# Performance work log

Measured on AMD Instinct MI355X. Metric: run time of the kernel, lower is better.

Reference implementation:

```python
import jax, jax.numpy as jnp
import numpy as np

N = 100000      # nodes
E = 800000      # edges
F_IN = 128      # input feature dim
HID = 8         # per-head hidden
HEADS = 8
HD = HID * HEADS  # 64
G = 128         # graphs in batch
C = 10          # classes
SLOPE = 0.2     # leaky relu negative slope


def setup_inputs() -> dict:
    key = jax.random.key(0)
    ks = iter(jax.random.split(key, 48))
    def rn(shape, scale=0.1):
        return jax.random.normal(next(ks), shape, jnp.float32) * scale
    inp = {
        'x': jax.random.normal(next(ks), (N, F_IN), jnp.float32),
        'edge_index': jax.random.randint(next(ks), (2, E), 0, N),
        'batch': jnp.sort(jax.random.randint(next(ks), (N,), 0, G)),
        # GAT layer 1
        'W1': rn((F_IN, HEADS * HID)), 'as1': rn((HEADS, HID)), 'ad1': rn((HEADS, HID)), 'b1': jnp.zeros((HEADS * HID,), jnp.float32),
        # GAT layer 2
        'W2': rn((HD, HEADS * HID)), 'as2': rn((HEADS, HID)), 'ad2': rn((HEADS, HID)), 'b2': jnp.zeros((HEADS * HID,), jnp.float32),
        # node attention MLP (HD -> HD//2 -> 2)
        'na_w1': rn((HD, HD // 2)), 'na_b1': jnp.zeros((HD // 2,), jnp.float32), 'na_w2': rn((HD // 2, 2)), 'na_b2': jnp.zeros((2,), jnp.float32),
        # edge attention MLP (2*HD -> HD -> 2)
        'ea_w1': rn((2 * HD, HD)), 'ea_b1': jnp.zeros((HD,), jnp.float32), 'ea_w2': rn((HD, 2)), 'ea_b2': jnp.zeros((2,), jnp.float32),
        # GCN causal / trivial
        'gc_w': rn((HD, HD)), 'gc_b': jnp.zeros((HD,), jnp.float32),
        'gt_w': rn((HD, HD)), 'gt_b': jnp.zeros((HD,), jnp.float32),
        # readouts
        'rc_w': rn((HD, HD)), 'rc_b': jnp.zeros((HD,), jnp.float32),
        'rt_w': rn((HD, HD)), 'rt_b': jnp.zeros((HD,), jnp.float32),
        # classifiers (HD -> HD//2 -> C), combined (2HD -> HD -> C)
        'cc_w1': rn((HD, HD // 2)), 'cc_b1': jnp.zeros((HD // 2,), jnp.float32), 'cc_w2': rn((HD // 2, C)), 'cc_b2': jnp.zeros((C,), jnp.float32),
        'ct_w1': rn((HD, HD // 2)), 'ct_b1': jnp.zeros((HD // 2,), jnp.float32), 'ct_w2': rn((HD // 2, C)), 'ct_b2': jnp.zeros((C,), jnp.float32),
        'cm_w1': rn((2 * HD, HD)), 'cm_b1': jnp.zeros((HD,), jnp.float32), 'cm_w2': rn((HD, C)), 'cm_b2': jnp.zeros((C,), jnp.float32),
    }
    return inp


def _mlp2(h, w1, b1, w2, b2):
    return jax.nn.relu(h @ w1 + b1) @ w2 + b2


def reference(x, edge_index, batch,
              W1, as1, ad1, b1, W2, as2, ad2, b2,
              na_w1, na_b1, na_w2, na_b2,
              ea_w1, ea_b1, ea_w2, ea_b2,
              gc_w, gc_b, gt_w, gt_b,
              rc_w, rc_b, rt_w, rt_b,
              cc_w1, cc_b1, cc_w2, cc_b2,
              ct_w1, ct_b1, ct_w2, ct_b2,
              cm_w1, cm_b1, cm_w2, cm_b2):
    src, dst = edge_index[0], edge_index[1]
    loop = jnp.arange(N)
    s2 = jnp.concatenate([src, loop])  # edges + self-loops (PyG GATConv/GCNConv add self-loops)
    d2 = jnp.concatenate([dst, loop])

    def gat(h_in, W, a_s, a_d, b):
        h = (h_in @ W).reshape(N, HEADS, HID)
        es = jnp.einsum('nhd,hd->nh', h, a_s)
        ed = jnp.einsum('nhd,hd->nh', h, a_d)
        logit = jax.nn.leaky_relu(es[s2] + ed[d2], SLOPE)      # [E+N, H]
        m = jax.ops.segment_max(logit, d2, num_segments=N)
        ex = jnp.exp(logit - m[d2])
        den = jax.ops.segment_sum(ex, d2, num_segments=N)
        alpha = ex / (den[d2] + 1e-16)
        out = jax.ops.segment_sum(h[s2] * alpha[..., None], d2, num_segments=N)
        return out.reshape(N, HEADS * HID) + b

    # GNN encoder (dropout disabled: eval mode)
    H1 = jax.nn.elu(gat(x, W1, as1, ad1, b1))
    H = gat(H1, W2, as2, ad2, b2)                              # [N, HD]

    # node attention
    na = jax.nn.softmax(_mlp2(H, na_w1, na_b1, na_w2, na_b2), axis=1)
    alpha_c, alpha_t = na[:, 0], na[:, 1]
    # edge attention (original edges, no self-loops)
    ef = jnp.concatenate([H[src], H[dst]], axis=1)             # [E, 2*HD]
    ea = jax.nn.softmax(_mlp2(ef, ea_w1, ea_b1, ea_w2, ea_b2), axis=1)
    beta_c, beta_t = ea[:, 0], ea[:, 1]

    Hc = H * alpha_c[:, None]
    Ht = H * alpha_t[:, None]

    def gcn(h_in, w, b, ew):
        # PyG gcn_norm: self-loops with weight 1, symmetric deg^-1/2 normalization
        w_full = jnp.concatenate([ew, jnp.ones((N,), h_in.dtype)])
        deg = jax.ops.segment_sum(w_full, d2, num_segments=N)
        dis = jnp.where(deg > 0, jax.lax.rsqrt(jnp.maximum(deg, 1e-20)), 0.0)
        norm = dis[s2] * w_full * dis[d2]
        h = h_in @ w
        return jax.ops.segment_sum(h[s2] * norm[:, None], d2, num_segments=N) + b

    Gc = gcn(Hc, gc_w, gc_b, beta_c)
    Gt = gcn(Ht, gt_w, gt_b, beta_t)

    # readout: linear then global_add_pool
    hGc = jax.ops.segment_sum(Gc @ rc_w + rc_b, batch, num_segments=G)  # [G, HD]
    hGt = jax.ops.segment_sum(Gt @ rt_w + rt_b, batch, num_segments=G)

    zc = _mlp2(hGc, cc_w1, cc_b1, cc_w2, cc_b2)
    zt = _mlp2(hGt, ct_w1, ct_b1, ct_w2, ct_b2)
    # RandomIntervention: within-graph node shuffle followed by add-pool == plain add-pool
    h_comb = jnp.concatenate([hGc + hGt], axis=1) if False else (hGc + hGt)
    zp = _mlp2(jnp.concatenate([h_comb, jnp.zeros_like(h_comb)], axis=1), cm_w1, cm_b1, cm_w2, cm_b2) if False else _mlp2_comb(h_comb, cm_w1, cm_b1, cm_w2, cm_b2)
    return (zc, zt, zp, hGc, hGt)


def _mlp2_comb(h_comb, cm_w1, cm_b1, cm_w2, cm_b2):
    # original: classifier_combined takes hidden_dim*2 input; forward feeds h_G_c + shuffled_h_G_t
    # which is [G, HD]; to match Linear(2*HD, ...) we use the first HD rows of cm_w1 twice?
    # NO -- the original code as written passes a [G, HD] tensor to a Linear(2*HD, HD) layer,
    # which would error in torch. Faithful runnable interpretation: combined feature is
    # concat([h_G_c, shuffled_h_G_t]) of width 2*HD (the standard CAL formulation).
    return jax.nn.relu(h_comb @ cm_w1 + cm_b1) @ cm_w2 + cm_b2


# clean final definition overriding the commented exploration above
def reference(x, edge_index, batch,
              W1, as1, ad1, b1, W2, as2, ad2, b2,
              na_w1, na_b1, na_w2, na_b2,
              ea_w1, ea_b1, ea_w2, ea_b2,
              gc_w, gc_b, gt_w, gt_b,
              rc_w, rc_b, rt_w, rt_b,
              cc_w1, cc_b1, cc_w2, cc_b2,
              ct_w1, ct_b1, ct_w2, ct_b2,
              cm_w1, cm_b1, cm_w2, cm_b2):
    src, dst = edge_index[0], edge_index[1]
    loop = jnp.arange(N)
    s2 = jnp.concatenate([src, loop])
    d2 = jnp.concatenate([dst, loop])

    def gat(h_in, W, a_s, a_d, b):
        h = (h_in @ W).reshape(N, HEADS, HID)
        es = jnp.einsum('nhd,hd->nh', h, a_s)
        ed = jnp.einsum('nhd,hd->nh', h, a_d)
        logit = jax.nn.leaky_relu(es[s2] + ed[d2], SLOPE)
        m = jax.ops.segment_max(logit, d2, num_segments=N)
        ex = jnp.exp(logit - m[d2])
        den = jax.ops.segment_sum(ex, d2, num_segments=N)
        alpha = ex / (den[d2] + 1e-16)
        out = jax.ops.segment_sum(h[s2] * alpha[..., None], d2, num_segments=N)
        return out.reshape(N, HEADS * HID) + b

    H1 = jax.nn.elu(gat(x, W1, as1, ad1, b1))
    H = gat(H1, W2, as2, ad2, b2)

    na = jax.nn.softmax(_mlp2(H, na_w1, na_b1, na_w2, na_b2), axis=1)
    alpha_c, alpha_t = na[:, 0], na[:, 1]
    ef = jnp.concatenate([H[src], H[dst]], axis=1)
    ea = jax.nn.softmax(_mlp2(ef, ea_w1, ea_b1, ea_w2, ea_b2), axis=1)
    beta_c, beta_t = ea[:, 0], ea[:, 1]

    Hc = H * alpha_c[:, None]
    Ht = H * alpha_t[:, None]

    def gcn(h_in, w, b, ew):
        w_full = jnp.concatenate([ew, jnp.ones((N,), h_in.dtype)])
        deg = jax.ops.segment_sum(w_full, d2, num_segments=N)
        dis = jnp.where(deg > 0, jax.lax.rsqrt(jnp.maximum(deg, 1e-20)), 0.0)
        norm = dis[s2] * w_full * dis[d2]
        h = h_in @ w
        return jax.ops.segment_sum(h[s2] * norm[:, None], d2, num_segments=N) + b

    Gc = gcn(Hc, gc_w, gc_b, beta_c)
    Gt = gcn(Ht, gt_w, gt_b, beta_t)

    hGc = jax.ops.segment_sum(Gc @ rc_w + rc_b, batch, num_segments=G)
    hGt = jax.ops.segment_sum(Gt @ rt_w + rt_b, batch, num_segments=G)

    zc = _mlp2(hGc, cc_w1, cc_b1, cc_w2, cc_b2)
    zt = _mlp2(hGt, ct_w1, ct_b1, ct_w2, ct_b2)
    # RandomIntervention with sorted batch: within-graph permutation + add-pool == add-pool
    h_comb = jnp.concatenate([hGc, hGt], axis=1)  # [G, 2*HD] for Linear(2*HD, ...)
    zp = _mlp2(h_comb, cm_w1, cm_b1, cm_w2, cm_b2)
    return (zc, zt, zp, hGc, hGt)


if __name__ == '__main__':
    out = reference(**setup_inputs())
    print([o.shape for o in out])
```

## Files before the change

kernel.cpp:

```cpp
#include <hip/hip_runtime.h>
#include <hip/hip_bf16.h>

#define N_NODES 100000
#define E_EDGES 800000
#define E2 (E_EDGES + N_NODES)
#define FIN 128
#define HD 64
#define NH 8
#define NG 128
#define NC 10
#define SLOPE 0.2f
#define SELF_FLAG 0x40000000
#define SRC_MASK  0x3FFFFFFF
#define NSCAN_BLK 391
#define NBLK64 1563
#define GB 16
#define ECAP 256
#define NPW 4
#define EA_BLKS 6250
#define AG_BLKS 6250

#define U1_STRIPES 261
#define U1_GRID (2 + U1_STRIPES * 7)
#define U1_HISTB (U1_STRIPES * 4)
#define T1 (U1_STRIPES * 3)
#define U2_STRIPES 391
#define U2_GRID (U2_STRIPES * 11)

typedef unsigned short bfu;

__device__ __forceinline__ float lrelu(float x) { return x > 0.f ? x : SLOPE * x; }

__device__ __forceinline__ bfu f2bf(float f) {
    unsigned int u = __float_as_uint(f);
    u += 0x7FFFu + ((u >> 16) & 1u);
    return (bfu)(u >> 16);
}
__device__ __forceinline__ float bf2f(bfu s) {
    return __uint_as_float(((unsigned int)s) << 16);
}
__device__ __forceinline__ float bflo(unsigned int u) { return __uint_as_float(u << 16); }
__device__ __forceinline__ float bfhi(unsigned int u) { return __uint_as_float(u & 0xFFFF0000u); }

template<typename TIN, int KIN, int MODE>
__device__ __forceinline__
void gemm_tile_body(float* smem, int tile,
                    const TIN* __restrict__ in, const float* __restrict__ W,
                    bfu* __restrict__ outB,
                    const float* __restrict__ a_s, const float* __restrict__ a_d,
                    float* __restrict__ es, float* __restrict__ ed)
{
    constexpr int KH = (KIN > 64) ? 64 : KIN;
    constexpr int RS = KIN + 4;
    float* Ws   = smem;
    float* rows = smem + KH * 64;
    int t = threadIdx.x;
    int base = tile * 64;

    if constexpr (sizeof(TIN) == 4) {
        constexpr int RQ = KIN / 4;
        for (int i = t; i < 64 * RQ; i += 256) {
            int r = i / RQ, c = (i % RQ) * 4;
            int n = base + r;
            float4 v = make_float4(0.f, 0.f, 0.f, 0.f);
            if (n < N_NODES) v = *(const float4*)((const float*)in + (size_t)n * KIN + c);
            *(float4*)(rows + r * RS + c) = v;
        }
    } else {
        constexpr int RQ = KIN / 8;
        for (int i = t; i < 64 * RQ; i += 256) {
            int r = i / RQ, c = (i % RQ) * 8;
            int n = base + r;
            uint4 v = make_uint4(0, 0, 0, 0);
// ... 19 lines not shown
        const float4* Wsv = (const float4*)Ws;
#pragma unroll 2
        for (int k = 0; k < KH; k += 4) {
            float4 w0 = Wsv[(k + 0) * 16 + tc];
            float4 w1 = Wsv[(k + 1) * 16 + tc];
            float4 w2 = Wsv[(k + 2) * 16 + tc];
            float4 w3 = Wsv[(k + 3) * 16 + tc];
            int kq = (h * KH + k) >> 2;
#pragma unroll
            for (int i = 0; i < 4; ++i) {
                float4 r = R4[(tr * 4 + i) * (RS / 4) + kq];
                acc[i][0] = fmaf(r.x, w0.x, fmaf(r.y, w1.x, fmaf(r.z, w2.x, fmaf(r.w, w3.x, acc[i][0]))));
                acc[i][1] = fmaf(r.x, w0.y, fmaf(r.y, w1.y, fmaf(r.z, w2.y, fmaf(r.w, w3.y, acc[i][1]))));
                acc[i][2] = fmaf(r.x, w0.z, fmaf(r.y, w1.z, fmaf(r.z, w2.z, fmaf(r.w, w3.z, acc[i][2]))));
                acc[i][3] = fmaf(r.x, w0.w, fmaf(r.y, w1.w, fmaf(r.z, w2.w, fmaf(r.w, w3.w, acc[i][3]))));
            }
        }
    }

    int j0 = tc * 4;
#pragma unroll
    for (int i = 0; i < 4; ++i) {
        int n = base + tr * 4 + i;
        if (n < N_NODES) {
            ushort4 ov;
            ov.x = f2bf(acc[i][0]); ov.y = f2bf(acc[i][1]);
            ov.z = f2bf(acc[i][2]); ov.w = f2bf(acc[i][3]);
            *(ushort4*)(outB + (size_t)n * 64 + j0) = ov;
        }
    }
    if (MODE == 1) {
        float s0[4], s1[4];
#pragma unroll
        for (int i = 0; i < 4; ++i) {
            float pes = 0.f, ped = 0.f;
#pragma unroll
            for (int q = 0; q < 4; ++q) {
                pes = fmaf(acc[i][q], a_s[j0 + q], pes);
                ped = fmaf(acc[i][q], a_d[j0 + q], ped);
            }
            pes += __shfl_xor(pes, 1, 64);
            ped += __shfl_xor(ped, 1, 64);
            s0[i] = pes; s1[i] = ped;
        }
        if ((tc & 1) == 0) {
            int h = tc >> 1;
#pragma unroll
            for (int i = 0; i < 4; ++i) {
                int n = base + tr * 4 + i;
                if (n < N_NODES) {
                    es[n * NH + h] = s0[i];
                    ed[n * NH + h] = s1[i];
                }
            }
        }
    }
}

__device__ __forceinline__
void weight_prep_body(float* smem,
                      const float* __restrict__ gw, const float* __restrict__ gb,
                      const float* __restrict__ rw, const float* __restrict__ rb,
                      float* __restrict__ Wp, float* __restrict__ bp)
{
    float* A = smem;
    float* B = smem + 4096;
    int t = threadIdx.x;
    {
        const float4* ga = (const float4*)gw;
        const float4* rA = (const float4*)rw;
        float4* dA = (float4*)A; float4* dB = (float4*)B;
        for (int i = t; i < 1024; i += 256) { dA[i] = ga[i]; dB[i] = rA[i]; }
    }
    __syncthreads();
    for (int e = t * 16; e < t * 16 + 16; ++e) {
        int k = e >> 6, j = e & 63;
        float acc = 0.f;
#pragma unroll 8
        for (int m = 0; m < 64; ++m) acc = fmaf(A[k * 64 + m], B[m * 64 + j], acc);
        Wp[e] = acc;
    }
    if (t < 64) {
        float acc = rb[t];
#pragma unroll 8
        for (int m = 0; m < 64; ++m) acc = fmaf(gb[m], B[m * 64 + t], acc);
        bp[t] = acc;
    }
}

__global__ __launch_bounds__(256)
void u1_fused(const float* __restrict__ x, const float* __restrict__ W1,
              bfu* __restrict__ B0, const float* __restrict__ as1,
              const float* __restrict__ ad1, float* __restrict__ es,
              float* __restrict__ ed,
              const int* __restrict__ ei, int* __restrict__ cnt,
              int* __restrict__ rank,
              const float* __restrict__ gc_w, const float* __restrict__ gc_b,
              const float* __restrict__ rc_w, const float* __restrict__ rc_b,
              const float* __restrict__ gt_w, const float* __restrict__ gt_b,
              const float* __restrict__ rt_w, const float* __restrict__ rt_b,
              float* __restrict__ Wcp, float* __restrict__ bcp,
              float* __restrict__ Wtp, float* __restrict__ btp)
{
    __shared__ __align__(16) float smem[12544];
    int b = blockIdx.x;
    if (b < 2) {
// ... 3 lines not shown
    }
    int u = b - 2;
    int stripe = u / 7, r = u % 7;
    if (r < 3) {
        gemm_tile_body<float, FIN, 1>(smem, stripe * 3 + r, x, W1, B0, as1, ad1, es, ed);
    } else {
        int idx = stripe * 4 + (r - 3);
        int t = threadIdx.x;
        const int STR = U1_HISTB * 256;
        for (int e = idx * 256 + t; e < E_EDGES; e += 2 * STR) {
            int e1 = e + STR;
            int d0 = ei[E_EDGES + e];
            int r0 = atomicAdd(&cnt[d0], 1);
            int r1 = 0;
            bool has1 = e1 < E_EDGES;
            if (has1) r1 = atomicAdd(&cnt[ei[E_EDGES + e1]], 1);
            rank[e] = r0;
            if (has1) rank[e1] = r1;
        }
    }
}

__global__ __launch_bounds__(256)
void u2_fused(const float* __restrict__ x, const float* __restrict__ W1,
              bfu* __restrict__ B0, const float* __restrict__ as1,
              const float* __restrict__ ad1, float* __restrict__ es,
              float* __restrict__ ed,
              const int* __restrict__ ei, const int* __restrict__ rank,
              const int* __restrict__ offs,
              int* __restrict__ csr)
{
    __shared__ __align__(16) float smem[12544];
    int b = blockIdx.x;
    int stripe = b / 11, r = b % 11;
    int t = threadIdx.x;
    if (r < 8) {
        int e = (stripe * 8 + r) * 256 + t;
        if (e < E_EDGES) {
            int s = ei[e], d = ei[E_EDGES + e];
            csr[offs[d] + rank[e]] = s;
        }
    } else if (r < 10) {
        int tile = T1 + stripe * 2 + (r - 8);
        if (tile < NBLK64)
            gemm_tile_body<float, FIN, 1>(smem, tile, x, W1, B0, as1, ad1, es, ed);
    } else {
        int n = stripe * 256 + t;
        if (n < N_NODES) {
            csr[offs[n + 1] - 1] = n | SELF_FLAG;
        }
    }
}

__global__ __launch_bounds__(256)
void u3_fused(const bfu* __restrict__ in,
              const float* __restrict__ na_w1, const float* __restrict__ na_b1,
              const float* __restrict__ na_w2, const float* __restrict__ na_b2,
              float2* __restrict__ al2,
              const float* __restrict__ ea_w1,
              bfu* __restrict__ out0, bfu* __restrict__ out1)
{
    __shared__ __align__(16) float smem[12544];
    float* Ws   = smem;
    float* rows = smem + 8192;
    int t = threadIdx.x;
    int base = blockIdx.x * 64;
    const float* W0 = ea_w1;
    const float* W1 = ea_w1 + 64 * 64;
    {
        const float4* W0v = (const float4*)W0;
        const float4* W1v = (const float4*)W1;
        float4* Wsv = (float4*)Ws;
        for (int i = t; i < 1024; i += 256) { Wsv[i] = W0v[i]; Wsv[1024 + i] = W1v[i]; }
    }
    for (int i = t; i < 64 * 8; i += 256) {
        int r = i >> 3, c = (i & 7) * 8;
        int n = base + r;
        uint4 v = make_uint4(0, 0, 0, 0);
        if (n < N_NODES) v = *(const uint4*)(in + (size_t)n * 64 + c);
        float* dp = rows + r * 68 + c;
        *(float4*)dp       = make_float4(bflo(v.x), bfhi(v.x), bflo(v.y), bfhi(v.y));
        *(float4*)(dp + 4) = make_float4(bflo(v.z), bfhi(v.z), bflo(v.w), bfhi(v.w));
    }
    __syncthreads();
    {
        int tr = t >> 4, tc = t & 15;
        float a0[4][4] = {}, a1[4][4] = {};
        const float4* Wsv = (const float4*)Ws;
        const float4* R4 = (const float4*)rows;
#pragma unroll 2
        for (int k = 0; k < 64; k += 4) {
            float4 p0 = Wsv[(k + 0) * 16 + tc];
            float4 p1 = Wsv[(k + 1) * 16 + tc];
            float4 p2 = Wsv[(k + 2) * 16 + tc];
            float4 p3 = Wsv[(k + 3) * 16 + tc];
            float4 q0 = Wsv[1024 + (k + 0) * 16 + tc];
            float4 q1 = Wsv[1024 + (k + 1) * 16 + tc];
            float4 q2 = Wsv[1024 + (k + 2) * 16 + tc];
            float4 q3 = Wsv[1024 + (k + 3) * 16 + tc];
            int kq = k >> 2;
#pragma unroll
            for (int i = 0; i < 4; ++i) {
                float4 r = R4[(tr * 4 + i) * 17 + kq];
                a0[i][0] = fmaf(r.x, p0.x, fmaf(r.y, p1.x, fmaf(r.z, p2.x, fmaf(r.w, p3.x, a0[i][0]))));
                a0[i][1] = fmaf(r.x, p0.y, fmaf(r.y, p1.y, fmaf(r.z, p2.y, fmaf(r.w, p3.y, a0[i][1]))));
                a0[i][2] = fmaf(r.x, p0.z, fmaf(r.y, p1.z, fmaf(r.z, p2.z, fmaf(r.w, p3.z, a0[i][2]))));
                a0[i][3] = fmaf(r.x, p0.w, fmaf(r.y, p1.w, fmaf(r.z, p2.w, fmaf(r.w, p3.w, a0[i][3]))));
                a1[i][0] = fmaf(r.x, q0.x, fmaf(r.y, q1.x, fmaf(r.z, q2.x, fmaf(r.w, q3.x, a1[i][0]))));
                a1[i][1] = fmaf(r.x, q0.y, fmaf(r.y, q1.y, fmaf(r.z, q2.y, fmaf(r.w, q3.y, a1[i][1]))));
                a1[i][2] = fmaf(r.x, q0.z, fmaf(r.y, q1.z, fmaf(r.z, q2.z, fmaf(r.w, q3.z, a1[i][2]))));
                a1[i][3] = fmaf(r.x, q0.w, fmaf(r.y, q1.w, fmaf(r.z, q2.w, fmaf(r.w, q3.w, a1[i][3]))));
            }
        }
        int j0 = tc * 4;
#pragma unroll
        for (int i = 0; i < 4; ++i) {
            int n = base + tr * 4 + i;
            if (n >= N_NODES) continue;
            ushort4 o0, o1;
            o0.x = f2bf(a0[i][0]); o0.y = f2bf(a0[i][1]);
            o0.z = f2bf(a0[i][2]); o0.w = f2bf(a0[i][3]);
            o1.x = f2bf(a1[i][0]); o1.y = f2bf(a1[i][1]);
            o1.z = f2bf(a1[i][2]); o1.w = f2bf(a1[i][3]);
            *(ushort4*)(out0 + (size_t)n * 64 + j0) = o0;
            *(ushort4*)(out1 + (size_t)n * 64 + j0) = o1;
        }
    }
    __syncthreads();
    {
        const float4* w1v = (const float4*)na_w1;
        float4* dst = (float4*)Ws;
        for (int i = t; i < 512; i += 256) dst[i] = w1v[i];
        if (t < 64) Ws[2048 + t] = na_w2[t];
    }
    __syncthreads();
    {
        int tr = t >> 3;
        int tc = t & 7;
        float4 bv = *(const float4*)(na_b1 + tc * 4);
        float4 acc0 = bv, acc1 = bv;
        const float4* w1sv = (const float4*)Ws;
#pragma unroll 8
        for (int k = 0; k < 64; ++k) {
            float4 w = w1sv[k * 8 + tc];
            float r0 = rows[tr * 68 + k];
            float r1 = rows[(tr + 32) * 68 + k];
            acc0.x = fmaf(r0, w.x, acc0.x); acc0.y = fmaf(r0, w.y, acc0.y);
            acc0.z = fmaf(r0, w.z, acc0.z); acc0.w = fmaf(r0, w.w, acc0.w);
            acc1.x = fmaf(r1, w.x, acc1.x); acc1.y = fmaf(r1, w.y, acc1.y);
            acc1.z = fmaf(r1, w.z, acc1.z); acc1.w = fmaf(r1, w.w, acc1.w);
        }
        float z00 = 0.f, z01 = 0.f, z10 = 0.f, z11 = 0.f;
        float h0, w20, w21;
        int j0 = tc * 4;
#pragma unroll
        for (int q = 0; q < 4; ++q) {
            float a0q = q == 0 ? acc0.x : q == 1 ? acc0.y : q == 2 ? acc0.z : acc0.w;
            float a1q = q == 0 ? acc1.x : q == 1 ? acc1.y : q == 2 ? acc1.z : acc1.w;
            w20 = Ws[2048 + (j0 + q) * 2]; w21 = Ws[2048 + (j0 + q) * 2 + 1];
            h0 = fmaxf(a0q, 0.f);
            z00 = fmaf(h0, w20, z00); z01 = fmaf(h0, w21, z01);
            h0 = fmaxf(a1q, 0.f);
            z10 = fmaf(h0, w20, z10); z11 = fmaf(h0, w21, z11);
        }
#pragma unroll
        for (int o = 1; o < 8; o <<= 1) {
            z00 += __shfl_xor(z00, o, 64); z01 += __shfl_xor(z01, o, 64);
            z10 += __shfl_xor(z10, o, 64); z11 += __shfl_xor(z11, o, 64);
        }
        if (tc == 0) {
            int n0 = base + tr, n1 = base + tr + 32;
            if (n0 < N_NODES) {
                float zz0 = z00 + na_b2[0], zz1 = z01 + na_b2[1];
                float mx = fmaxf(zz0, zz1);
                float e0 = __expf(zz0 - mx), e1 = __expf(zz1 - mx);
                float ss = e0 + e1;
                al2[n0] = make_float2(e0 / ss, e1 / ss);
            }
            if (n1 < N_NODES) {
                float zz0 = z10 + na_b2[0], zz1 = z11 + na_b2[1];
                float mx = fmaxf(zz0, zz1);
                float e0 = __expf(zz0 - mx), e1 = __expf(zz1 - mx);
                float ss = e0 + e1;
                al2[n1] = make_float2(e0 / ss, e1 / ss);
            }
        }
    }
}

__global__ __launch_bounds__(256)
void gemm_tile_k64(const bfu* __restrict__ in, const float* __restrict__ W,
                   bfu* __restrict__ outB,
                   const float* __restrict__ a_s, const float* __restrict__ a_d,
                   float* __restrict__ es, float* __restrict__ ed)
{
    __shared__ __align__(16) float smem[64 * 64 + 64 * 68];
    gemm_tile_body<bfu, 64, 1>(smem, blockIdx.x, in, W, outB, a_s, a_d, es, ed);
}

__global__ void csr_scan1(const int* __restrict__ cnt, int* __restrict__ offs,
                          int* __restrict__ bsum, const int* __restrict__ batch,
                          int* __restrict__ glo)
{
    __shared__ int tmp[256];
    int t = threadIdx.x;
    int i = blockIdx.x * 256 + t;
    int v = (i < N_NODES) ? cnt[i] + 1 : 0;
    tmp[t] = v; __syncthreads();
#pragma unroll
    for (int o = 1; o < 256; o <<= 1) {
        int a = (t >= o) ? tmp[t - o] : 0;
        __syncthreads();
        tmp[t] += a;
        __syncthreads();
    }
    if (i < N_NODES) offs[i] = tmp[t] - v;
    if (t == 255) bsum[blockIdx.x] = tmp[255];
    if (blockIdx.x == 0 && t <= NG) {
        int l = 0, r = N_NODES;
        while (l < r) { int m = (l + r) >> 1; if (batch[m] < t) l = m + 1; else r = m; }
        glo[t] = l;
    }
}

__global__ void csr_scan23(int* __restrict__ offs, const int* __restrict__ bsum)
{
    __shared__ int tmp[256];
    int b = blockIdx.x;
    int t = threadIdx.x;
    int s = 0;
    for (int j = t; j < b; j += 256) s += bsum[j];
    tmp[t] = s; __syncthreads();
#pragma unroll
    for (int o = 128; o > 0; o >>= 1) {
        if (t < o) tmp[t] += tmp[t + o];
        __syncthreads();
    }
    int prefix = tmp[0];
    int i = b * 256 + t;
    if (i < N_NODES) offs[i] += prefix;
    if (i == 0) offs[N_NODES] = E2;
}

template<int ELU>
__global__ void gat_aggregate4(const int* __restrict__ offs, const int* __restrict__ csr,
                               const float* __restrict__ es, const float* __restrict__ ed,
                               const bfu* __restrict__ hsrcB, const float* __restrict__ bias,
                               bfu* __restrict__ outB)
{
    int w = threadIdx.x >> 6;
    int lane = threadIdx.x & 63;
    int slot = lane >> 4;
    int fl = lane & 15;
    int h  = fl >> 1;
    int n = (blockIdx.x * 4 + w) * 4 + slot;
    if (n >= N_NODES) return;
    float4 bv = *(const float4*)(bias + fl * 4);
    int beg = offs[n], end = offs[n + 1];
    float edv = ed[n * NH + h];
    float den = 0.f;
    float4 acc = make_float4(0.f, 0.f, 0.f, 0.f);
    int p = beg;
    for (; p + 1 < end; p += 2) {
        int s0 = csr[p] & SRC_MASK;
        int s1 = csr[p + 1] & SRC_MASK;
        float ex0 = __expf(lrelu(es[s0 * NH + h] + edv));
        float ex1 = __expf(lrelu(es[s1 * NH + h] + edv));
        den += ex0 + ex1;
        ushort4 ra = *(const ushort4*)(hsrcB + (size_t)s0 * HD + fl * 4);
        ushort4 rb = *(const ushort4*)(hsrcB + (size_t)s1 * HD + fl * 4);
        acc.x = fmaf(bf2f(ra.x), ex0, fmaf(bf2f(rb.x), ex1, acc.x));
        acc.y = fmaf(bf2f(ra.y), ex0, fmaf(bf2f(rb.y), ex1, acc.y));
        acc.z = fmaf(bf2f(ra.z), ex0, fmaf(bf2f(rb.z), ex1, acc.z));
        acc.w = fmaf(bf2f(ra.w), ex0, fmaf(bf2f(rb.w), ex1, acc.w));
    }
    if (p < end) {
        int s = csr[p] & SRC_MASK;
        float ex = __expf(lrelu(es[s * NH + h] + edv));
        den += ex;
        ushort4 rb = *(const ushort4*)(hsrcB + (size_t)s * HD + fl * 4);
        acc.x = fmaf(bf2f(rb.x), ex, acc.x);
        acc.y = fmaf(bf2f(rb.y), ex, acc.y);
        acc.z = fmaf(bf2f(rb.z), ex, acc.z);
        acc.w = fmaf(bf2f(rb.w), ex, acc.w);
    }
    float inv = 1.f / (den + 1e-16f);
    float v0 = acc.x * inv + bv.x;
    float v1 = acc.y * inv + bv.y;
    float v2 = acc.z * inv + bv.z;
    float v3 = acc.w * inv + bv.w;
    if (ELU) {
        v0 = v0 > 0.f ? v0 : (__expf(v0) - 1.f);
        v1 = v1 > 0.f ? v1 : (__expf(v1) - 1.f);
        v2 = v2 > 0.f ? v2 : (__expf(v2) - 1.f);
        v3 = v3 > 0.f ? v3 : (__expf(v3) - 1.f);
    }
    ushort4 ov;
    ov.x = f2bf(v0); ov.y = f2bf(v1); ov.z = f2bf(v2); ov.w = f2bf(v3);
    *(ushort4*)(outB + (size_t)n * HD + fl * 4) = ov;
}

__global__ __launch_bounds__(256)
void edge_att_node(const int* __restrict__ offs, const int* __restrict__ csr,
                   const bfu* __restrict__ P1b, const bfu* __restrict__ P2b,
                   const float* __restrict__ b1, const float* __restrict__ w2,
                   const float* __restrict__ b2,
                   const float2* __restrict__ al2,
                   float2* __restrict__ beta2,
                   float2* __restrict__ prod2)
{
    __shared__ float2 bbuf[4][ECAP];
    int w = threadIdx.x >> 6;
    int lane = threadIdx.x & 63;
    int nbase = (blockIdx.x * 4 + w) * NPW;
    if (nbase >= N_NODES) return;
    int slot = lane >> 3, q = lane & 7;
    const float4* pb = (const float4*)(b1 + q * 8);
    const float4* pw = (const float4*)(w2 + q * 16);
    float4 c0 = pb[0], c1 = pb[1];
    float4 w0 = pw[0], w1v = pw[1], w2v = pw[2], w3v = pw[3];
    float wd0 = w0.x - w0.y,   wd1 = w0.z - w0.w;
    float wd2 = w1v.x - w1v.y, wd3 = w1v.z - w1v.w;
    float wd4 = w2v.x - w2v.y, wd5 = w2v.z - w2v.w;
    float wd6 = w3v.x - w3v.y, wd7 = w3v.z - w3v.w;
    float zbd = b2[0] - b2[1];
    for (int j = 0; j < NPW; ++j) {
        int n = nbase + j;
        if (n >= N_NODES) return;
        uint4 U2 = *(const uint4*)(P2b + (size_t)n * 64 + q * 8);
        float d0 = bflo(U2.x) + c0.x, d1 = bfhi(U2.x) + c0.y;
        float d2 = bflo(U2.y) + c0.z, d3 = bfhi(U2.y) + c0.w;
        float d4 = bflo(U2.z) + c1.x, d5 = bfhi(U2.z) + c1.y;
        float d6 = bflo(U2.w) + c1.z, d7 = bfhi(U2.w) + c1.w;
        int beg = offs[n], endr = offs[n + 1] - 1;
        int m = endr - beg;
        float dc = 0.f, dt = 0.f;
        for (int p = beg + slot; p < endr; p += 8) {
            int s = csr[p];
            uint4 U1 = *(const uint4*)(P1b + (size_t)s * 64 + q * 8);
            float h0 = fmaxf(bflo(U1.x) + d0, 0.f);
            float h1 = fmaxf(bfhi(U1.x) + d1, 0.f);
            float h2 = fmaxf(bflo(U1.y) + d2, 0.f);
            float h3 = fmaxf(bfhi(U1.y) + d3, 0.f);
            float h4 = fmaxf(bflo(U1.z) + d4, 0.f);
            float h5 = fmaxf(bfhi(U1.z) + d5, 0.f);
            float h6 = fmaxf(bflo(U1.w) + d6, 0.f);
            float h7 = fmaxf(bfhi(U1.w) + d7, 0.f);
            float z = fmaf(h0, wd0, fmaf(h1, wd1, fmaf(h2, wd2, fmaf(h3, wd3,
                      fmaf(h4, wd4, fmaf(h5, wd5, fmaf(h6, wd6, h7 * wd7)))))));
            z += __shfl_xor(z, 1, 64);
            z += __shfl_xor(z, 2, 64);
            z += __shfl_xor(z, 4, 64);
// ... 196 lines not shown
    const float* na_b1 = (const float*)d_in[12];
    const float* na_w2 = (const float*)d_in[13];
    const float* na_b2 = (const float*)d_in[14];
    const float* ea_w1 = (const float*)d_in[15];
    const float* ea_b1 = (const float*)d_in[16];
    const float* ea_w2 = (const float*)d_in[17];
    const float* ea_b2 = (const float*)d_in[18];
    const float* gc_w  = (const float*)d_in[19];
    const float* gc_b  = (const float*)d_in[20];
    const float* gt_w  = (const float*)d_in[21];
    const float* gt_b  = (const float*)d_in[22];
    const float* rc_w  = (const float*)d_in[23];
    const float* rc_b  = (const float*)d_in[24];
    const float* rt_w  = (const float*)d_in[25];
    const float* rt_b  = (const float*)d_in[26];
    const float* cc_w1 = (const float*)d_in[27];
    const float* cc_b1 = (const float*)d_in[28];
    const float* cc_w2 = (const float*)d_in[29];
    const float* cc_b2 = (const float*)d_in[30];
    const float* ct_w1 = (const float*)d_in[31];
    const float* ct_b1 = (const float*)d_in[32];
    const float* ct_w2 = (const float*)d_in[33];
    const float* ct_b2 = (const float*)d_in[34];
    const float* cm_w1 = (const float*)d_in[35];
    const float* cm_b1 = (const float*)d_in[36];
    const float* cm_w2 = (const float*)d_in[37];
    const float* cm_b2 = (const float*)d_in[38];
    float* out = (float*)d_out;

    float* ws = (float*)d_ws;
    size_t o = 0;
    const size_t nf = (size_t)N_NODES * HD;
    float* es    = ws + o; o += (size_t)N_NODES * NH;
    float* ed    = ws + o; o += (size_t)N_NODES * NH;
    float2* al2  = (float2*)(ws + o); o += (size_t)N_NODES * 2;
    float2* beta2= (float2*)(ws + o); o += (size_t)E2 * 2;
    float2* prod2= (float2*)(ws + o); o += (size_t)N_NODES * 2;
    bfu* B0      = (bfu*)(ws + o); o += nf / 2;
    bfu* B1      = (bfu*)(ws + o); o += nf / 2;
    bfu* B2      = (bfu*)(ws + o); o += nf / 2;
    bfu* BH1     = (bfu*)(ws + o); o += nf / 2;
    int* csr     = (int*)(ws + o); o += E2;
    int* offs    = (int*)(ws + o); o += N_NODES + 1;
    float* Pc    = ws + o; o += (size_t)NG * GB * 64;
    float* Pt    = ws + o; o += (size_t)NG * GB * 64;
    float* Wcp   = ws + o; o += 4096;
    float* Wtp   = ws + o; o += 4096;
    float* bcp   = ws + o; o += 64;
    float* btp   = ws + o; o += 64;
    int* glo     = (int*)(ws + o); o += NG + 2;
    int* cnt  = (int*)beta2;
    int* bsum = (int*)prod2;
    int* rank = (int*)B1;

    hipMemsetAsync(cnt, 0, (size_t)N_NODES * 4, stream);
    u1_fused<<<U1_GRID, 256, 0, stream>>>(x, W1, B0, as1, ad1, es, ed,
                                          ei, cnt, rank,
                                          gc_w, gc_b, rc_w, rc_b,
                                          gt_w, gt_b, rt_w, rt_b,
                                          Wcp, bcp, Wtp, btp);
    csr_scan1<<<NSCAN_BLK, 256, 0, stream>>>(cnt, offs, bsum, batch, glo);
    csr_scan23<<<NSCAN_BLK, 256, 0, stream>>>(offs, bsum);

    u2_fused<<<U2_GRID, 256, 0, stream>>>(x, W1, B0, as1, ad1, es, ed,
                                          ei, rank, offs, csr);

    gat_aggregate4<1><<<AG_BLKS, 256, 0, stream>>>(offs, csr, es, ed, B0, b1, BH1);

    gemm_tile_k64<<<NBLK64, 256, 0, stream>>>(BH1, W2, B0, as2, ad2, es, ed);
    gat_aggregate4<0><<<AG_BLKS, 256, 0, stream>>>(offs, csr, es, ed, B0, b2, B2);

    u3_fused<<<NBLK64, 256, 0, stream>>>(B2, na_w1, na_b1, na_w2, na_b2, al2,
                                         ea_w1, B0, B1);

    edge_att_node<<<EA_BLKS, 256, 0, stream>>>(offs, csr, B0, B1,
                                               ea_b1, ea_w2, ea_b2, al2,
                                               beta2, prod2);

    gcn_readout_fused<<<NG * GB, 256, 0, stream>>>(offs, csr, glo, B2,
                                                   beta2, prod2, Pc, Pt);

    head_final<<<NG, 64, 0, stream>>>(Pc, Pt, glo,
                                      Wcp, bcp, Wtp, btp,
                                      cc_w1, cc_b1, cc_w2, cc_b2,
                                      ct_w1, ct_b1, ct_w2, ct_b2,
                                      cm_w1, cm_b1, cm_w2, cm_b2, out);
    (void)in_sizes; (void)n_in; (void)out_size; (void)ws_size;
}
```

Baseline: 446.0 us.

## Fuse GAT aggregation with following dense projections into two kernels

Merges layer-1 GAT aggregation with the layer-2 linear projection and attention-score computation, and merges layer-2 aggregation with the edge-attention projection and node-attention MLP. Aggregated rows stay in shared memory as fp32 instead of round-tripping through global bf16 buffers, which removes two launches and the intermediate reads and writes. es2/ed2 live in the beta2 workspace to avoid overwriting es/ed while they are still being read. Each block now does the irregular gather and the GEMM serially, so the fused kernels carry a larger shared-memory footprint and load imbalance from high-degree nodes may stall the whole tile.

```diff
diff --git a/kernel.cpp b/kernel.cpp
--- a/kernel.cpp
+++ b/kernel.cpp
@@ -18,7 +18,6 @@
 #define ECAP 256
 #define NPW 4
 #define EA_BLKS 6250
-#define AG_BLKS 6250
 
 #define U1_STRIPES 261
 #define U1_GRID (2 + U1_STRIPES * 7)
@@ -144,6 +143,283 @@
                     es[n * NH + h] = s0[i];
                     ed[n * NH + h] = s1[i];
                 }
+            }
+        }
+    }
+}
+
+template<int ELU, int GSTORE>
+__device__ __forceinline__
+void agg_phase(float* rows, int base,
+               const int* __restrict__ offs, const int* __restrict__ csr,
+               const float* __restrict__ es, const float* __restrict__ ed,
+               const bfu* __restrict__ hsrcB, const float* __restrict__ bias,
+               bfu* __restrict__ outB)
+{
+    int t = threadIdx.x;
+    int w = t >> 6, lane = t & 63;
+    int slot = lane >> 4, fl = lane & 15, h = fl >> 1;
+    float4 bv = *(const float4*)(bias + fl * 4);
+#pragma unroll
+    for (int jj = 0; jj < 4; ++jj) {
+        int local = w * 16 + jj * 4 + slot;
+        int n = base + local;
+        if (n >= N_NODES) {
+            *(float4*)(rows + local * 68 + fl * 4) = make_float4(0.f, 0.f, 0.f, 0.f);
+            continue;
+        }
+        int beg = offs[n], end = offs[n + 1];
+        float edv = ed[n * NH + h];
+        float den = 0.f;
+        float4 acc = make_float4(0.f, 0.f, 0.f, 0.f);
+        int p = beg;
+        for (; p + 1 < end; p += 2) {
+            int s0 = csr[p] & SRC_MASK;
+            int s1 = csr[p + 1] & SRC_MASK;
+            float ex0 = __expf(lrelu(es[s0 * NH + h] + edv));
+            float ex1 = __expf(lrelu(es[s1 * NH + h] + edv));
+            den += ex0 + ex1;
+            ushort4 ra = *(const ushort4*)(hsrcB + (size_t)s0 * HD + fl * 4);
+            ushort4 rb = *(const ushort4*)(hsrcB + (size_t)s1 * HD + fl * 4);
+            acc.x = fmaf(bf2f(ra.x), ex0, fmaf(bf2f(rb.x), ex1, acc.x));
+            acc.y = fmaf(bf2f(ra.y), ex0, fmaf(bf2f(rb.y), ex1, acc.y));
+            acc.z = fmaf(bf2f(ra.z), ex0, fmaf(bf2f(rb.z), ex1, acc.z));
+            acc.w = fmaf(bf2f(ra.w), ex0, fmaf(bf2f(rb.w), ex1, acc.w));
+        }
+        if (p < end) {
+            int s = csr[p] & SRC_MASK;
+            float ex = __expf(lrelu(es[s * NH + h] + edv));
+            den += ex;
+            ushort4 rb = *(const ushort4*)(hsrcB + (size_t)s * HD + fl * 4);
+            acc.x = fmaf(bf2f(rb.x), ex, acc.x);
+            acc.y = fmaf(bf2f(rb.y), ex, acc.y);
+            acc.z = fmaf(bf2f(rb.z), ex, acc.z);
+            acc.w = fmaf(bf2f(rb.w), ex, acc.w);
+        }
+        float inv = 1.f / (den + 1e-16f);
+        float v0 = acc.x * inv + bv.x;
+        float v1 = acc.y * inv + bv.y;
+        float v2 = acc.z * inv + bv.z;
+        float v3 = acc.w * inv + bv.w;
+        if (ELU) {
+            v0 = v0 > 0.f ? v0 : (__expf(v0) - 1.f);
+            v1 = v1 > 0.f ? v1 : (__expf(v1) - 1.f);
+            v2 = v2 > 0.f ? v2 : (__expf(v2) - 1.f);
+            v3 = v3 > 0.f ? v3 : (__expf(v3) - 1.f);
+        }
+        *(float4*)(rows + local * 68 + fl * 4) = make_float4(v0, v1, v2, v3);
+        if (GSTORE) {
+            ushort4 ov;
+            ov.x = f2bf(v0); ov.y = f2bf(v1); ov.z = f2bf(v2); ov.w = f2bf(v3);
+            *(ushort4*)(outB + (size_t)n * HD + fl * 4) = ov;
+        }
+    }
+}
+
+__global__ __launch_bounds__(256)
+void agg1_gemm2(const int* __restrict__ offs, const int* __restrict__ csr,
+                const float* __restrict__ es, const float* __restrict__ ed,
+                const bfu* __restrict__ B0, const float* __restrict__ b1,
+                const float* __restrict__ W2,
+                bfu* __restrict__ outB ,
+                const float* __restrict__ as2, const float* __restrict__ ad2,
+                float* __restrict__ es2, float* __restrict__ ed2)
+{
+    __shared__ __align__(16) float smem[4096 + 64 * 68];
+    float* Ws   = smem;
+    float* rows = smem + 4096;
+    int t = threadIdx.x;
+    int base = blockIdx.x * 64;
+    {
+        const float4* Wv = (const float4*)W2;
+        float4* Wsv4 = (float4*)Ws;
+        for (int i = t; i < 1024; i += 256) Wsv4[i] = Wv[i];
+    }
+    agg_phase<1, 0>(rows, base, offs, csr, es, ed, B0, b1, nullptr);
+    __syncthreads();
+    int tr = t >> 4, tc = t & 15;
+    float acc[4][4] = {};
+    const float4* R4 = (const float4*)rows;
+    const float4* Wsv = (const float4*)Ws;
+#pragma unroll 2
+    for (int k = 0; k < 64; k += 4) {
+        float4 w0 = Wsv[(k + 0) * 16 + tc];
+        float4 w1 = Wsv[(k + 1) * 16 + tc];
+        float4 w2 = Wsv[(k + 2) * 16 + tc];
+        float4 w3 = Wsv[(k + 3) * 16 + tc];
+        int kq = k >> 2;
+#pragma unroll
+        for (int i = 0; i < 4; ++i) {
+            float4 r = R4[(tr * 4 + i) * 17 + kq];
+            acc[i][0] = fmaf(r.x, w0.x, fmaf(r.y, w1.x, fmaf(r.z, w2.x, fmaf(r.w, w3.x, acc[i][0]))));
+            acc[i][1] = fmaf(r.x, w0.y, fmaf(r.y, w1.y, fmaf(r.z, w2.y, fmaf(r.w, w3.y, acc[i][1]))));
+            acc[i][2] = fmaf(r.x, w0.z, fmaf(r.y, w1.z, fmaf(r.z, w2.z, fmaf(r.w, w3.z, acc[i][2]))));
+            acc[i][3] = fmaf(r.x, w0.w, fmaf(r.y, w1.w, fmaf(r.z, w2.w, fmaf(r.w, w3.w, acc[i][3]))));
+        }
+    }
+    int j0 = tc * 4;
+#pragma unroll
+    for (int i = 0; i < 4; ++i) {
+        int n = base + tr * 4 + i;
+        if (n < N_NODES) {
+            ushort4 ov;
+            ov.x = f2bf(acc[i][0]); ov.y = f2bf(acc[i][1]);
+            ov.z = f2bf(acc[i][2]); ov.w = f2bf(acc[i][3]);
+            *(ushort4*)(outB + (size_t)n * 64 + j0) = ov;
+        }
+    }
+    {
+        float s0[4], s1[4];
+#pragma unroll
+        for (int i = 0; i < 4; ++i) {
+            float pes = 0.f, ped = 0.f;
+#pragma unroll
+            for (int q = 0; q < 4; ++q) {
+                pes = fmaf(acc[i][q], as2[j0 + q], pes);
+                ped = fmaf(acc[i][q], ad2[j0 + q], ped);
+            }
+            pes += __shfl_xor(pes, 1, 64);
+            ped += __shfl_xor(ped, 1, 64);
+            s0[i] = pes; s1[i] = ped;
+        }
+        if ((tc & 1) == 0) {
+            int h = tc >> 1;
+#pragma unroll
+            for (int i = 0; i < 4; ++i) {
+                int n = base + tr * 4 + i;
+                if (n < N_NODES) {
+                    es2[n * NH + h] = s0[i];
+                    ed2[n * NH + h] = s1[i];
+                }
+            }
+        }
+    }
+}
+
+__global__ __launch_bounds__(256)
+void agg2_proj(const int* __restrict__ offs, const int* __restrict__ csr,
+               const float* __restrict__ es2, const float* __restrict__ ed2,
+               const bfu* __restrict__ BH1, const float* __restrict__ b2,
+               bfu* __restrict__ B2,
+               const float* __restrict__ ea_w1,
+               bfu* __restrict__ P1, bfu* __restrict__ P2,
+               const float* __restrict__ na_w1, const float* __restrict__ na_b1,
+               const float* __restrict__ na_w2, const float* __restrict__ na_b2,
+               float2* __restrict__ al2)
+{
+    __shared__ __align__(16) float smem[12544];
+    float* Ws   = smem;
+    float* rows = smem + 8192;
+    int t = threadIdx.x;
+    int base = blockIdx.x * 64;
+    {
+        const float4* W0v = (const float4*)ea_w1;
+        const float4* W1v = (const float4*)(ea_w1 + 64 * 64);
+        float4* Wsv = (float4*)Ws;
+        for (int i = t; i < 1024; i += 256) { Wsv[i] = W0v[i]; Wsv[1024 + i] = W1v[i]; }
+    }
+    agg_phase<0, 1>(rows, base, offs, csr, es2, ed2, BH1, b2, B2);
+    __syncthreads();
+    {
+        int tr = t >> 4, tc = t & 15;
+        float a0[4][4] = {}, a1[4][4] = {};
+        const float4* Wsv = (const float4*)Ws;
+        const float4* R4 = (const float4*)rows;
+#pragma unroll 2
+        for (int k = 0; k < 64; k += 4) {
+            float4 p0 = Wsv[(k + 0) * 16 + tc];
+            float4 p1 = Wsv[(k + 1) * 16 + tc];
+            float4 p2 = Wsv[(k + 2) * 16 + tc];
+            float4 p3 = Wsv[(k + 3) * 16 + tc];
+            float4 q0 = Wsv[1024 + (k + 0) * 16 + tc];
+            float4 q1 = Wsv[1024 + (k + 1) * 16 + tc];
+            float4 q2 = Wsv[1024 + (k + 2) * 16 + tc];
+            float4 q3 = Wsv[1024 + (k + 3) * 16 + tc];
+            int kq = k >> 2;
+#pragma unroll
+            for (int i = 0; i < 4; ++i) {
+                float4 r = R4[(tr * 4 + i) * 17 + kq];
+                a0[i][0] = fmaf(r.x, p0.x, fmaf(r.y, p1.x, fmaf(r.z, p2.x, fmaf(r.w, p3.x, a0[i][0]))));
+                a0[i][1] = fmaf(r.x, p0.y, fmaf(r.y, p1.y, fmaf(r.z, p2.y, fmaf(r.w, p3.y, a0[i][1]))));
+                a0[i][2] = fmaf(r.x, p0.z, fmaf(r.y, p1.z, fmaf(r.z, p2.z, fmaf(r.w, p3.z, a0[i][2]))));
+                a0[i][3] = fmaf(r.x, p0.w, fmaf(r.y, p1.w, fmaf(r.z, p2.w, fmaf(r.w, p3.w, a0[i][3]))));
+                a1[i][0] = fmaf(r.x, q0.x, fmaf(r.y, q1.x, fmaf(r.z, q2.x, fmaf(r.w, q3.x, a1[i][0]))));
+                a1[i][1] = fmaf(r.x, q0.y, fmaf(r.y, q1.y, fmaf(r.z, q2.y, fmaf(r.w, q3.y, a1[i][1]))));
+                a1[i][2] = fmaf(r.x, q0.z, fmaf(r.y, q1.z, fmaf(r.z, q2.z, fmaf(r.w, q3.z, a1[i][2]))));
+                a1[i][3] = fmaf(r.x, q0.w, fmaf(r.y, q1.w, fmaf(r.z, q2.w, fmaf(r.w, q3.w, a1[i][3]))));
+            }
+        }
+        int j0 = tc * 4;
+#pragma unroll
+        for (int i = 0; i < 4; ++i) {
+            int n = base + tr * 4 + i;
+            if (n >= N_NODES) continue;
+            ushort4 o0, o1;
+            o0.x = f2bf(a0[i][0]); o0.y = f2bf(a0[i][1]);
+            o0.z = f2bf(a0[i][2]); o0.w = f2bf(a0[i][3]);
+            o1.x = f2bf(a1[i][0]); o1.y = f2bf(a1[i][1]);
+            o1.z = f2bf(a1[i][2]); o1.w = f2bf(a1[i][3]);
+            *(ushort4*)(P1 + (size_t)n * 64 + j0) = o0;
+            *(ushort4*)(P2 + (size_t)n * 64 + j0) = o1;
+        }
+    }
+    __syncthreads();
+    {
+        const float4* w1v = (const float4*)na_w1;
+        float4* dst = (float4*)Ws;
+        for (int i = t; i < 512; i += 256) dst[i] = w1v[i];
+        if (t < 64) Ws[2048 + t] = na_w2[t];
+    }
+    __syncthreads();
+    {
+        int tr = t >> 3;
+        int tc = t & 7;
+        float4 bv = *(const float4*)(na_b1 + tc * 4);
+        float4 acc0 = bv, acc1 = bv;
+        const float4* w1sv = (const float4*)Ws;
+#pragma unroll 8
+        for (int k = 0; k < 64; ++k) {
+            float4 w = w1sv[k * 8 + tc];
+            float r0 = rows[tr * 68 + k];
+            float r1 = rows[(tr + 32) * 68 + k];
+            acc0.x = fmaf(r0, w.x, acc0.x); acc0.y = fmaf(r0, w.y, acc0.y);
+            acc0.z = fmaf(r0, w.z, acc0.z); acc0.w = fmaf(r0, w.w, acc0.w);
+            acc1.x = fmaf(r1, w.x, acc1.x); acc1.y = fmaf(r1, w.y, acc1.y);
+            acc1.z = fmaf(r1, w.z, acc1.z); acc1.w = fmaf(r1, w.w, acc1.w);
+        }
+        float z00 = 0.f, z01 = 0.f, z10 = 0.f, z11 = 0.f;
+        float h0, w20, w21;
+        int j0 = tc * 4;
+#pragma unroll
+        for (int q = 0; q < 4; ++q) {
+            float a0q = q == 0 ? acc0.x : q == 1 ? acc0.y : q == 2 ? acc0.z : acc0.w;
+            float a1q = q == 0 ? acc1.x : q == 1 ? acc1.y : q == 2 ? acc1.z : acc1.w;
+            w20 = Ws[2048 + (j0 + q) * 2]; w21 = Ws[2048 + (j0 + q) * 2 + 1];
+            h0 = fmaxf(a0q, 0.f);
+            z00 = fmaf(h0, w20, z00); z01 = fmaf(h0, w21, z01);
+            h0 = fmaxf(a1q, 0.f);
+            z10 = fmaf(h0, w20, z10); z11 = fmaf(h0, w21, z11);
+        }
+#pragma unroll
+        for (int o = 1; o < 8; o <<= 1) {
+            z00 += __shfl_xor(z00, o, 64); z01 += __shfl_xor(z01, o, 64);
+            z10 += __shfl_xor(z10, o, 64); z11 += __shfl_xor(z11, o, 64);
+        }
+        if (tc == 0) {
+            int n0 = base + tr, n1 = base + tr + 32;
+            if (n0 < N_NODES) {
+                float zz0 = z00 + na_b2[0], zz1 = z01 + na_b2[1];
+                float mx = fmaxf(zz0, zz1);
+                float e0 = __expf(zz0 - mx), e1 = __expf(zz1 - mx);
+                float ss = e0 + e1;
+                al2[n0] = make_float2(e0 / ss, e1 / ss);
+            }
+            if (n1 < N_NODES) {
+                float zz0 = z10 + na_b2[0], zz1 = z11 + na_b2[1];
+                float mx = fmaxf(zz0, zz1);
+                float e0 = __expf(zz0 - mx), e1 = __expf(zz1 - mx);
+                float ss = e0 + e1;
+                al2[n1] = make_float2(e0 / ss, e1 / ss);
             }
         }
     }
@@ -253,152 +529,6 @@
     }
 }
 
-__global__ __launch_bounds__(256)
-void u3_fused(const bfu* __restrict__ in,
-              const float* __restrict__ na_w1, const float* __restrict__ na_b1,
-              const float* __restrict__ na_w2, const float* __restrict__ na_b2,
-              float2* __restrict__ al2,
-              const float* __restrict__ ea_w1,
-              bfu* __restrict__ out0, bfu* __restrict__ out1)
-{
-    __shared__ __align__(16) float smem[12544];
-    float* Ws   = smem;
-    float* rows = smem + 8192;
-    int t = threadIdx.x;
-    int base = blockIdx.x * 64;
-    const float* W0 = ea_w1;
-    const float* W1 = ea_w1 + 64 * 64;
-    {
-        const float4* W0v = (const float4*)W0;
-        const float4* W1v = (const float4*)W1;
-        float4* Wsv = (float4*)Ws;
-        for (int i = t; i < 1024; i += 256) { Wsv[i] = W0v[i]; Wsv[1024 + i] = W1v[i]; }
-    }
-    for (int i = t; i < 64 * 8; i += 256) {
-        int r = i >> 3, c = (i & 7) * 8;
-        int n = base + r;
-        uint4 v = make_uint4(0, 0, 0, 0);
-        if (n < N_NODES) v = *(const uint4*)(in + (size_t)n * 64 + c);
-        float* dp = rows + r * 68 + c;
-        *(float4*)dp       = make_float4(bflo(v.x), bfhi(v.x), bflo(v.y), bfhi(v.y));
-        *(float4*)(dp + 4) = make_float4(bflo(v.z), bfhi(v.z), bflo(v.w), bfhi(v.w));
-    }
-    __syncthreads();
-    {
-        int tr = t >> 4, tc = t & 15;
-        float a0[4][4] = {}, a1[4][4] = {};
-        const float4* Wsv = (const float4*)Ws;
-        const float4* R4 = (const float4*)rows;
-#pragma unroll 2
-        for (int k = 0; k < 64; k += 4) {
-            float4 p0 = Wsv[(k + 0) * 16 + tc];
-            float4 p1 = Wsv[(k + 1) * 16 + tc];
-            float4 p2 = Wsv[(k + 2) * 16 + tc];
-            float4 p3 = Wsv[(k + 3) * 16 + tc];
-            float4 q0 = Wsv[1024 + (k + 0) * 16 + tc];
-            float4 q1 = Wsv[1024 + (k + 1) * 16 + tc];
-            float4 q2 = Wsv[1024 + (k + 2) * 16 + tc];
-            float4 q3 = Wsv[1024 + (k + 3) * 16 + tc];
-            int kq = k >> 2;
-#pragma unroll
-            for (int i = 0; i < 4; ++i) {
-                float4 r = R4[(tr * 4 + i) * 17 + kq];
-                a0[i][0] = fmaf(r.x, p0.x, fmaf(r.y, p1.x, fmaf(r.z, p2.x, fmaf(r.w, p3.x, a0[i][0]))));
-                a0[i][1] = fmaf(r.x, p0.y, fmaf(r.y, p1.y, fmaf(r.z, p2.y, fmaf(r.w, p3.y, a0[i][1]))));
-                a0[i][2] = fmaf(r.x, p0.z, fmaf(r.y, p1.z, fmaf(r.z, p2.z, fmaf(r.w, p3.z, a0[i][2]))));
-                a0[i][3] = fmaf(r.x, p0.w, fmaf(r.y, p1.w, fmaf(r.z, p2.w, fmaf(r.w, p3.w, a0[i][3]))));
-                a1[i][0] = fmaf(r.x, q0.x, fmaf(r.y, q1.x, fmaf(r.z, q2.x, fmaf(r.w, q3.x, a1[i][0]))));
-                a1[i][1] = fmaf(r.x, q0.y, fmaf(r.y, q1.y, fmaf(r.z, q2.y, fmaf(r.w, q3.y, a1[i][1]))));
-                a1[i][2] = fmaf(r.x, q0.z, fmaf(r.y, q1.z, fmaf(r.z, q2.z, fmaf(r.w, q3.z, a1[i][2]))));
-                a1[i][3] = fmaf(r.x, q0.w, fmaf(r.y, q1.w, fmaf(r.z, q2.w, fmaf(r.w, q3.w, a1[i][3]))));
-            }
-        }
-        int j0 = tc * 4;
-#pragma unroll
-        for (int i = 0; i < 4; ++i) {
-            int n = base + tr * 4 + i;
-            if (n >= N_NODES) continue;
-            ushort4 o0, o1;
-            o0.x = f2bf(a0[i][0]); o0.y = f2bf(a0[i][1]);
-            o0.z = f2bf(a0[i][2]); o0.w = f2bf(a0[i][3]);
-            o1.x = f2bf(a1[i][0]); o1.y = f2bf(a1[i][1]);
-            o1.z = f2bf(a1[i][2]); o1.w = f2bf(a1[i][3]);
-            *(ushort4*)(out0 + (size_t)n * 64 + j0) = o0;
-            *(ushort4*)(out1 + (size_t)n * 64 + j0) = o1;
-        }
-    }
-    __syncthreads();
-    {
-        const float4* w1v = (const float4*)na_w1;
-        float4* dst = (float4*)Ws;
-        for (int i = t; i < 512; i += 256) dst[i] = w1v[i];
-        if (t < 64) Ws[2048 + t] = na_w2[t];
-    }
-    __syncthreads();
-    {
-        int tr = t >> 3;
-        int tc = t & 7;
-        float4 bv = *(const float4*)(na_b1 + tc * 4);
-        float4 acc0 = bv, acc1 = bv;
-        const float4* w1sv = (const float4*)Ws;
-#pragma unroll 8
-        for (int k = 0; k < 64; ++k) {
-            float4 w = w1sv[k * 8 + tc];
-            float r0 = rows[tr * 68 + k];
-            float r1 = rows[(tr + 32) * 68 + k];
-            acc0.x = fmaf(r0, w.x, acc0.x); acc0.y = fmaf(r0, w.y, acc0.y);
-            acc0.z = fmaf(r0, w.z, acc0.z); acc0.w = fmaf(r0, w.w, acc0.w);
-            acc1.x = fmaf(r1, w.x, acc1.x); acc1.y = fmaf(r1, w.y, acc1.y);
-            acc1.z = fmaf(r1, w.z, acc1.z); acc1.w = fmaf(r1, w.w, acc1.w);
-        }
-        float z00 = 0.f, z01 = 0.f, z10 = 0.f, z11 = 0.f;
-        float h0, w20, w21;
-        int j0 = tc * 4;
-#pragma unroll
-        for (int q = 0; q < 4; ++q) {
-            float a0q = q == 0 ? acc0.x : q == 1 ? acc0.y : q == 2 ? acc0.z : acc0.w;
-            float a1q = q == 0 ? acc1.x : q == 1 ? acc1.y : q == 2 ? acc1.z : acc1.w;
-            w20 = Ws[2048 + (j0 + q) * 2]; w21 = Ws[2048 + (j0 + q) * 2 + 1];
-            h0 = fmaxf(a0q, 0.f);
-            z00 = fmaf(h0, w20, z00); z01 = fmaf(h0, w21, z01);
-            h0 = fmaxf(a1q, 0.f);
-            z10 = fmaf(h0, w20, z10); z11 = fmaf(h0, w21, z11);
-        }
-#pragma unroll
-        for (int o = 1; o < 8; o <<= 1) {
-            z00 += __shfl_xor(z00, o, 64); z01 += __shfl_xor(z01, o, 64);
-            z10 += __shfl_xor(z10, o, 64); z11 += __shfl_xor(z11, o, 64);
-        }
-        if (tc == 0) {
-            int n0 = base + tr, n1 = base + tr + 32;
-            if (n0 < N_NODES) {
-                float zz0 = z00 + na_b2[0], zz1 = z01 + na_b2[1];
-                float mx = fmaxf(zz0, zz1);
-                float e0 = __expf(zz0 - mx), e1 = __expf(zz1 - mx);
-                float ss = e0 + e1;
-                al2[n0] = make_float2(e0 / ss, e1 / ss);
-            }
-            if (n1 < N_NODES) {
-                float zz0 = z10 + na_b2[0], zz1 = z11 + na_b2[1];
-                float mx = fmaxf(zz0, zz1);
-                float e0 = __expf(zz0 - mx), e1 = __expf(zz1 - mx);
-                float ss = e0 + e1;
-                al2[n1] = make_float2(e0 / ss, e1 / ss);
-            }
-        }
-    }
-}
-
-__global__ __launch_bounds__(256)
-void gemm_tile_k64(const bfu* __restrict__ in, const float* __restrict__ W,
-                   bfu* __restrict__ outB,
-                   const float* __restrict__ a_s, const float* __restrict__ a_d,
-                   float* __restrict__ es, float* __restrict__ ed)
-{
-    __shared__ __align__(16) float smem[64 * 64 + 64 * 68];
-    gemm_tile_body<bfu, 64, 1>(smem, blockIdx.x, in, W, outB, a_s, a_d, es, ed);
-}
-
 __global__ void csr_scan1(const int* __restrict__ cnt, int* __restrict__ offs,
                           int* __restrict__ bsum, const int* __restrict__ batch,
                           int* __restrict__ glo)
@@ -441,64 +571,6 @@
     int i = b * 256 + t;
     if (i < N_NODES) offs[i] += prefix;
     if (i == 0) offs[N_NODES] = E2;
-}
-
-template<int ELU>
-__global__ void gat_aggregate4(const int* __restrict__ offs, const int* __restrict__ csr,
-                               const float* __restrict__ es, const float* __restrict__ ed,
-                               const bfu* __restrict__ hsrcB, const float* __restrict__ bias,
-                               bfu* __restrict__ outB)
-{
-    int w = threadIdx.x >> 6;
-    int lane = threadIdx.x & 63;
-    int slot = lane >> 4;
-    int fl = lane & 15;
-    int h  = fl >> 1;
-    int n = (blockIdx.x * 4 + w) * 4 + slot;
-    if (n >= N_NODES) return;
-    float4 bv = *(const float4*)(bias + fl * 4);
-    int beg = offs[n], end = offs[n + 1];
-    float edv = ed[n * NH + h];
-    float den = 0.f;
-    float4 acc = make_float4(0.f, 0.f, 0.f, 0.f);
-    int p = beg;
-    for (; p + 1 < end; p += 2) {
-        int s0 = csr[p] & SRC_MASK;
-        int s1 = csr[p + 1] & SRC_MASK;
-        float ex0 = __expf(lrelu(es[s0 * NH + h] + edv));
-        float ex1 = __expf(lrelu(es[s1 * NH + h] + edv));
-        den += ex0 + ex1;
-        ushort4 ra = *(const ushort4*)(hsrcB + (size_t)s0 * HD + fl * 4);
-        ushort4 rb = *(const ushort4*)(hsrcB + (size_t)s1 * HD + fl * 4);
-        acc.x = fmaf(bf2f(ra.x), ex0, fmaf(bf2f(rb.x), ex1, acc.x));
-        acc.y = fmaf(bf2f(ra.y), ex0, fmaf(bf2f(rb.y), ex1, acc.y));
-        acc.z = fmaf(bf2f(ra.z), ex0, fmaf(bf2f(rb.z), ex1, acc.z));
-        acc.w = fmaf(bf2f(ra.w), ex0, fmaf(bf2f(rb.w), ex1, acc.w));
-    }
-    if (p < end) {
-        int s = csr[p] & SRC_MASK;
-        float ex = __expf(lrelu(es[s * NH + h] + edv));
-        den += ex;
-        ushort4 rb = *(const ushort4*)(hsrcB + (size_t)s * HD + fl * 4);
-        acc.x = fmaf(bf2f(rb.x), ex, acc.x);
-        acc.y = fmaf(bf2f(rb.y), ex, acc.y);
-        acc.z = fmaf(bf2f(rb.z), ex, acc.z);
-        acc.w = fmaf(bf2f(rb.w), ex, acc.w);
-    }
-    float inv = 1.f / (den + 1e-16f);
-    float v0 = acc.x * inv + bv.x;
-    float v1 = acc.y * inv + bv.y;
-    float v2 = acc.z * inv + bv.z;
-    float v3 = acc.w * inv + bv.w;
-    if (ELU) {
-        v0 = v0 > 0.f ? v0 : (__expf(v0) - 1.f);
-        v1 = v1 > 0.f ? v1 : (__expf(v1) - 1.f);
-        v2 = v2 > 0.f ? v2 : (__expf(v2) - 1.f);
-        v3 = v3 > 0.f ? v3 : (__expf(v3) - 1.f);
-    }
-    ushort4 ov;
-    ov.x = f2bf(v0); ov.y = f2bf(v1); ov.z = f2bf(v2); ov.w = f2bf(v3);
-    *(ushort4*)(outB + (size_t)n * HD + fl * 4) = ov;
 }
 
 __global__ __launch_bounds__(256)
@@ -801,6 +873,8 @@
     int* cnt  = (int*)beta2;
     int* bsum = (int*)prod2;
     int* rank = (int*)B1;
+    float* es2 = (float*)beta2;
+    float* ed2 = es2 + (size_t)N_NODES * NH;
 
     hipMemsetAsync(cnt, 0, (size_t)N_NODES * 4, stream);
     u1_fused<<<U1_GRID, 256, 0, stream>>>(x, W1, B0, as1, ad1, es, ed,
@@ -814,13 +888,12 @@
     u2_fused<<<U2_GRID, 256, 0, stream>>>(x, W1, B0, as1, ad1, es, ed,
                                           ei, rank, offs, csr);
 
-    gat_aggregate4<1><<<AG_BLKS, 256, 0, stream>>>(offs, csr, es, ed, B0, b1, BH1);
-
-    gemm_tile_k64<<<NBLK64, 256, 0, stream>>>(BH1, W2, B0, as2, ad2, es, ed);
-    gat_aggregate4<0><<<AG_BLKS, 256, 0, stream>>>(offs, csr, es, ed, B0, b2, B2);
-
-    u3_fused<<<NBLK64, 256, 0, stream>>>(B2, na_w1, na_b1, na_w2, na_b2, al2,
-                                         ea_w1, B0, B1);
+    agg1_gemm2<<<NBLK64, 256, 0, stream>>>(offs, csr, es, ed, B0, b1,
+                                           W2, BH1, as2, ad2, es2, ed2);
+
+    agg2_proj<<<NBLK64, 256, 0, stream>>>(offs, csr, es2, ed2, BH1, b2,
+                                          B2, ea_w1, B0, B1,
+                                          na_w1, na_b1, na_w2, na_b2, al2);
 
     edge_att_node<<<EA_BLKS, 256, 0, stream>>>(offs, csr, B0, B1,
                                                ea_b1, ea_w2, ea_b2, al2,
```

Result: slower. 480.1 us (+7.6%).
